# Optimization experiments

Hardware: AMD Instinct MI355X
Metric: run time of the kernel (lower is better)

## Reference

```python
import jax, jax.numpy as jnp
import numpy as np

B, H, M = 8192, 1024, 4096


def setup_inputs() -> dict:
    key = jax.random.key(0)
    ks = jax.random.split(key, 5)
    s = 1.0 / np.sqrt(H)  # keep projections well-scaled
    return {
        "x": jax.random.normal(ks[0], (B, H), dtype=jnp.float32),
        "memory_bank": jax.random.normal(ks[1], (M, H), dtype=jnp.float32),
        "Wq": jax.random.normal(ks[2], (H, H), dtype=jnp.float32) * s,
        "bq": jnp.zeros((H,), dtype=jnp.float32),
        "Wk": jax.random.normal(ks[3], (H, H), dtype=jnp.float32) * s,
        "bk": jnp.zeros((H,), dtype=jnp.float32),
        "Wv": jax.random.normal(ks[4], (H, H), dtype=jnp.float32) * s,
        "bv": jnp.zeros((H,), dtype=jnp.float32),
    }


def reference(x, memory_bank, Wq, bq, Wk, bk, Wv, bv):
    # Dense projections (Keras Dense: y = x @ W + b)
    query = x @ Wq + bq                    # [B, H]
    keys = memory_bank @ Wk + bk           # [M, H]
    values = memory_bank @ Wv + bv         # [M, H]
    d_k = jnp.asarray(keys.shape[-1], dtype=query.dtype)
    scores = (query @ keys.T) / jnp.sqrt(d_k)   # [B, M]
    weights = jax.nn.softmax(scores, axis=-1)   # softmax over memory slots
    memory_context = weights @ values           # [B, H]
    return x + memory_context
```

## Files before the change

kernel.cpp:

```cpp
#include <hip/hip_runtime.h>
#include <stdint.h>

typedef unsigned short u16;
typedef unsigned char u8;
using f32x4 = __attribute__((ext_vector_type(4))) float;
using i32x4 = __attribute__((ext_vector_type(4))) int;
using i32x8 = __attribute__((ext_vector_type(8))) int;

__device__ __forceinline__ void gload_lds16(const void* g, void* l) {
  __builtin_amdgcn_global_load_lds(
      (const __attribute__((address_space(1))) void*)g,
      (__attribute__((address_space(3))) void*)l, 16, 0, 0);
}

#define DSRO(dst, base, offbytes) \
  asm volatile("ds_read_b128 %0, %1 offset:%2" : "=v"(dst) : "v"(base), "i"(offbytes))

__device__ __forceinline__ u8 f2fp8(float v) {
  return (u8)((uint32_t)__builtin_amdgcn_cvt_pk_fp8_f32(v, 0.f, 0, false) & 0xff);
}

__global__ __launch_bounds__(256) void cast_fp8_kernel(
    const float* __restrict__ in, u8* __restrict__ out, int n8) {
  int idx = blockIdx.x * blockDim.x + threadIdx.x;
  int stride = gridDim.x * blockDim.x;
  for (int i = idx; i < n8; i += stride) {
    const float4* p = (const float4*)(in + (size_t)i * 8);
    float4 a = p[0], b = p[1];
    uint32_t w0 = (uint32_t)__builtin_amdgcn_cvt_pk_fp8_f32(a.x, a.y, 0, false);
    w0 = (uint32_t)__builtin_amdgcn_cvt_pk_fp8_f32(a.z, a.w, (int)w0, true);
    uint32_t w1 = (uint32_t)__builtin_amdgcn_cvt_pk_fp8_f32(b.x, b.y, 0, false);
    w1 = (uint32_t)__builtin_amdgcn_cvt_pk_fp8_f32(b.z, b.w, (int)w1, true);
    uint2 o; o.x = w0; o.y = w1;
    *(uint2*)(out + (size_t)i * 8) = o;
  }
}

__global__ __launch_bounds__(256) void tcast_fp8_kernel(
    const float* __restrict__ W, u8* __restrict__ Wt, int Kd, int Nd) {
  __shared__ u8 tile[32][33];
  int nbx = Nd / 32;
  int bx = blockIdx.x % nbx;
  int by = blockIdx.x / nbx;
  int tr = threadIdx.x >> 5;
  int tc = threadIdx.x & 31;
#pragma unroll
  for (int i = 0; i < 4; ++i)
    tile[tr + i * 8][tc] = f2fp8(W[(size_t)(by * 32 + tr + i * 8) * Nd + bx * 32 + tc]);
  __syncthreads();
#pragma unroll
  for (int i = 0; i < 4; ++i)
    Wt[(size_t)(bx * 32 + tr + i * 8) * Kd + by * 32 + tc] = tile[tc][tr + i * 8];
}

#define GATE0 asm volatile("s_waitcnt vmcnt(0)" ::: "memory")
#define LGKM0 asm volatile("s_waitcnt lgkmcnt(0)" ::: "memory")
#define SBARA asm volatile("s_barrier" ::: "memory")
#define SCHED0 __builtin_amdgcn_sched_barrier(0)
#define NOSTG (void)0
#define NOTAIL (void)0
#define TAIL_G0 do { GATE0; SBARA; } while (0)

#define PVSTG(buf, kt) do { \
    const u8* sa_ = Asrc + (size_t)(kt) * 128; \
    gload_lds16(sa_,                    &As8[buf][wave * 1024]); \
    gload_lds16(sa_ + (size_t)64 * Kd,  &As8[buf][wave * 1024 + 8192]); \
    gload_lds16(sa_ + (size_t)128 * Kd, &As8[buf][wave * 1024 + 16384]); \
    gload_lds16(sa_ + (size_t)192 * Kd, &As8[buf][wave * 1024 + 24576]); \
    const u8* sb_ = Bsrc + (size_t)(kt) * 128; \
    gload_lds16(sb_,                    &Bs8[buf][wave * 1024]); \
    gload_lds16(sb_ + (size_t)64 * Kd,  &Bs8[buf][wave * 1024 + 8192]); \
  } while (0)

#define PVPH(buf, STAGE, TAIL) do { \
    i32x4 alo[4], ahi[4], blo[4], bhi[4]; \
    _Pragma("unroll") \
    for (int q = 0; q < 4; ++q) { \
      DSRO(alo[q], pvA[buf], q * 2048); \
      DSRO(ahi[q], pvA2[buf], q * 2048); \
      DSRO(blo[q], pvB[buf], q * 2048); \
      DSRO(bhi[q], pvB2[buf], q * 2048); \
    } \
    STAGE; \
    LGKM0; \
    SCHED0; \
    __builtin_amdgcn_s_setprio(1); \
    _Pragma("unroll") \
    for (int i2 = 0; i2 < 4; ++i2) { \
      i32x8 av = __builtin_shufflevector(alo[i2], ahi[i2], 0, 1, 2, 3, 4, 5, 6, 7); \
      _Pragma("unroll") \
      for (int j2 = 0; j2 < 4; ++j2) { \
        i32x8 bv = __builtin_shufflevector(blo[j2], bhi[j2], 0, 1, 2, 3, 4, 5, 6, 7); \
        acc[i2][j2] = __builtin_amdgcn_mfma_scale_f32_16x16x128_f8f6f4( \
            av, bv, acc[i2][j2], 0, 0, 0, 127, 0, 127); \
      } \
    } \
    __builtin_amdgcn_s_setprio(0); \
    SCHED0; \
    TAIL; \
  } while (0)

#define FP8GEMM_SETUP \
  int tid = threadIdx.x; \
  int lane = tid & 63; \
  int wave = tid >> 6; \
  int wm = (wave >> 1) * 64; \
  int wn = (wave & 1) * 64; \
  int laneh = lane & 15; \
  int lanev = lane >> 4; \
  int prow = tid >> 3; \
  int lslot = (tid & 7) ^ (prow & 7); \
  const u8* Asrc = A + (m0 + prow) * Kd + lslot * 16; \
  const u8* Bsrc = Bt + (n0 + prow) * Kd + lslot * 16; \
  int arow = wm + laneh; \
  int brow = wn + laneh; \
  uint32_t pvA[2], pvA2[2], pvB[2], pvB2[2]; \
  _Pragma("unroll") \
  for (int b = 0; b < 2; ++b) { \
    pvA[b]  = (uint32_t)(uintptr_t)&As8[b][arow * 128 + (((2 * lanev) ^ (arow & 7)) * 16)]; \
    pvA2[b] = (uint32_t)(uintptr_t)&As8[b][arow * 128 + (((2 * lanev + 1) ^ (arow & 7)) * 16)]; \
    pvB[b]  = (uint32_t)(uintptr_t)&Bs8[b][brow * 128 + (((2 * lanev) ^ (brow & 7)) * 16)]; \
    pvB2[b] = (uint32_t)(uintptr_t)&Bs8[b][brow * 128 + (((2 * lanev + 1) ^ (brow & 7)) * 16)]; \
  }

#define FP8GEMM_MAIN \
  PVSTG(0, 0); \
  GATE0; \
  SBARA; \
  int NI = Kd >> 7; \
  for (int it = 0; it < (NI >> 1) - 1; ++it) { \
    PVPH(0, PVSTG(1, 2 * it + 1), TAIL_G0); \
    PVPH(1, PVSTG(0, 2 * it + 2), TAIL_G0); \
  } \
  PVPH(0, PVSTG(1, NI - 1), TAIL_G0); \
  PVPH(1, NOSTG, NOTAIL);

#define EPI_FP8_FLAT(DST, BIAS) do { \
    int crow = (int)m0 + wm + (lanev << 2); \
    int ccol = (int)n0 + wn + laneh; \
    _Pragma("unroll") \
    for (int mi = 0; mi < 4; ++mi) \
      _Pragma("unroll") \
      for (int r = 0; r < 4; ++r) { \
        size_t row = (size_t)(crow + mi * 16 + r); \
        float v0 = acc[mi][0][r] + BIAS[ccol]; \
        float v1 = acc[mi][1][r] + BIAS[ccol + 16]; \
        float v2 = acc[mi][2][r] + BIAS[ccol + 32]; \
        float v3 = acc[mi][3][r] + BIAS[ccol + 48]; \
        uint32_t p01 = (uint32_t)__builtin_amdgcn_cvt_pk_fp8_f32(v0, v1, 0, false); \
        uint32_t p23 = (uint32_t)__builtin_amdgcn_cvt_pk_fp8_f32(v2, v3, 0, false); \
        size_t base = row * N + ccol; \
        DST[base]      = (u8)(p01 & 0xff); \
        DST[base + 16] = (u8)((p01 >> 8) & 0xff); \
        DST[base + 32] = (u8)(p23 & 0xff); \
        DST[base + 48] = (u8)((p23 >> 8) & 0xff); \
      } \
  } while (0)

__global__ __launch_bounds__(512, 2) void gemm_q8(
    const u8* __restrict__ A, const u8* __restrict__ Bt, u8* __restrict__ C,
    const float* __restrict__ bias, int M, int N, int Kd) {
  __shared__ u8 As8[2][256 * 128];
  __shared__ u8 Bs8[2][128 * 128];

  int bid = blockIdx.x;
  int bm = (bid & 7) * 4 + ((bid >> 3) & 3);
  int bn = bid >> 5;
  size_t m0 = (size_t)bm << 8;
  size_t n0 = (size_t)bn << 7;

  FP8GEMM_SETUP
  f32x4 acc[4][4] = {};
  FP8GEMM_MAIN
  EPI_FP8_FLAT(C, bias);
}

__global__ __launch_bounds__(512, 2) void gemm_kv8(
    const u8* __restrict__ mb8, const u8* __restrict__ Wkt8,
    const u8* __restrict__ Wvt8, u8* __restrict__ K8, u8* __restrict__ Vt8,
    const float* __restrict__ bk, const float* __restrict__ bv,
    int M, int N, int Kd) {
  __shared__ u8 As8[2][256 * 128];
  __shared__ u8 Bs8[2][128 * 128];

  int bid = blockIdx.x;
  int role = bid >> 7;
  int local = bid & 127;
  int bm = local & 15;
  int bn = local >> 4;
  size_t m0 = (size_t)bm << 8;
  size_t n0 = (size_t)bn << 7;

  const u8* A = mb8;
  const u8* Bt = role ? Wvt8 : Wkt8;

  FP8GEMM_SETUP
  f32x4 acc[4][4] = {};
  FP8GEMM_MAIN

  if (role == 0) {
    EPI_FP8_FLAT(K8, bk);
  } else {
    int crow = (int)m0 + wm + (lanev << 2);
    int ccol = (int)n0 + wn + laneh;
#pragma unroll
    for (int ni = 0; ni < 4; ++ni) {
      float b = bv[ccol + ni * 16];
#pragma unroll
      for (int mi = 0; mi < 4; ++mi) {
        uint32_t w = (uint32_t)__builtin_amdgcn_cvt_pk_fp8_f32(
            acc[mi][ni][0] + b, acc[mi][ni][1] + b, 0, false);
        w = (uint32_t)__builtin_amdgcn_cvt_pk_fp8_f32(
            acc[mi][ni][2] + b, acc[mi][ni][3] + b, (int)w, true);
        *(uint32_t*)&Vt8[(size_t)(ccol + ni * 16) * M + crow + mi * 16] = w;
      }
    }
  }
}

__global__ __launch_bounds__(512, 2) void gemm_qkt8(
    const u8* __restrict__ A, const u8* __restrict__ Bt, u8* __restrict__ C,
    float* __restrict__ sums, int M, int N, int Kd) {
  __shared__ u8 As8[2][256 * 128];
  __shared__ u8 Bs8[2][128 * 128];

  int bid = blockIdx.x;
  int bm = (bid & 7) * 4 + ((bid >> 3) & 3);
  int bn = bid >> 5;
  size_t m0 = (size_t)bm << 8;
  size_t n0 = (size_t)bn << 7;

  FP8GEMM_SETUP
  f32x4 acc[4][4] = {};
  FP8GEMM_MAIN

  SBARA;

  u8* epw = ((u8*)As8) + wave * 4608;
  int gcol0 = (int)n0 + wn;
#pragma unroll
  for (int mi = 0; mi < 4; ++mi)
#pragma unroll
    for (int r = 0; r < 4; ++r) {
      int rowL = mi * 16 + lanev * 4 + r;
      float e0 = __expf(acc[mi][0][r] * 0.03125f);
      float e1 = __expf(acc[mi][1][r] * 0.03125f);
      float e2 = __expf(acc[mi][2][r] * 0.03125f);
      float e3 = __expf(acc[mi][3][r] * 0.03125f);
      uint32_t p01 = (uint32_t)__builtin_amdgcn_cvt_pk_fp8_f32(e0, e1, 0, false);
      uint32_t p23 = (uint32_t)__builtin_amdgcn_cvt_pk_fp8_f32(e2, e3, 0, false);
      int base = rowL * 72 + laneh;
      epw[base]      = (u8)(p01 & 0xff);
      epw[base + 16] = (u8)((p01 >> 8) & 0xff);
      epw[base + 32] = (u8)(p23 & 0xff);
      epw[base + 48] = (u8)((p23 >> 8) & 0xff);
    }
#pragma unroll
  for (int p = 0; p < 4; ++p) {
    int rowL = (lane >> 2) + 16 * p;
    uint4 v = *(const uint4*)&epw[rowL * 72 + (lane & 3) * 16];
    size_t grow = m0 + wm + rowL;
    *(uint4*)&C[grow * N + gcol0 + (lane & 3) * 16] = v;
    float s = 0.f;
    s += __builtin_amdgcn_cvt_f32_fp8((int)v.x, 0);
    s += __builtin_amdgcn_cvt_f32_fp8((int)v.x, 1);
    s += __builtin_amdgcn_cvt_f32_fp8((int)v.x, 2);
    s += __builtin_amdgcn_cvt_f32_fp8((int)v.x, 3);
    s += __builtin_amdgcn_cvt_f32_fp8((int)v.y, 0);
    s += __builtin_amdgcn_cvt_f32_fp8((int)v.y, 1);
    s += __builtin_amdgcn_cvt_f32_fp8((int)v.y, 2);
    s += __builtin_amdgcn_cvt_f32_fp8((int)v.y, 3);
    s += __builtin_amdgcn_cvt_f32_fp8((int)v.z, 0);
    s += __builtin_amdgcn_cvt_f32_fp8((int)v.z, 1);
    s += __builtin_amdgcn_cvt_f32_fp8((int)v.z, 2);
    s += __builtin_amdgcn_cvt_f32_fp8((int)v.z, 3);
    s += __builtin_amdgcn_cvt_f32_fp8((int)v.w, 0);
    s += __builtin_amdgcn_cvt_f32_fp8((int)v.w, 1);
    s += __builtin_amdgcn_cvt_f32_fp8((int)v.w, 2);
    s += __builtin_amdgcn_cvt_f32_fp8((int)v.w, 3);
    s += __shfl_xor(s, 1, 64);
    s += __shfl_xor(s, 2, 64);
    if ((lane & 3) == 0) atomicAdd(&sums[grow], s);
  }
}

__global__ __launch_bounds__(512, 2) void gemm_pv_fp8(
    const u8* __restrict__ A, const u8* __restrict__ Bt,
    float* __restrict__ C, const float* __restrict__ sums,
    const float* __restrict__ xres, int M, int N, int Kd) {
  __shared__ u8 As8[2][256 * 128];
  __shared__ u8 Bs8[2][128 * 128];

  int bid = blockIdx.x;
  int bm = (bid & 7) * 4 + ((bid >> 3) & 3);
  int bn = bid >> 5;
  size_t m0 = (size_t)bm << 8;
  size_t n0 = (size_t)bn << 7;

  FP8GEMM_SETUP
  f32x4 acc[4][4] = {};
  FP8GEMM_MAIN

  int crow = (int)m0 + wm + (lanev << 2);
  int ccol = (int)n0 + wn + laneh;
#pragma unroll
  for (int mi = 0; mi < 4; ++mi)
#pragma unroll
    for (int r = 0; r < 4; ++r) {
      int row = crow + mi * 16 + r;
      float inv = 1.0f / sums[row];
      size_t rbase = (size_t)row * N + ccol;
#pragma unroll
      for (int ni = 0; ni < 4; ++ni)
        C[rbase + ni * 16] = xres[rbase + ni * 16] + acc[mi][ni][r] * inv;
    }
}

extern "C" void kernel_launch(void* const* d_in, const int* in_sizes, int n_in,
                              void* d_out, int out_size, void* d_ws, size_t ws_size,
                              hipStream_t stream) {
  const float* x  = (const float*)d_in[0];
  const float* mb = (const float*)d_in[1];
  const float* Wq = (const float*)d_in[2];
  const float* bq = (const float*)d_in[3];
  const float* Wk = (const float*)d_in[4];
  const float* bk = (const float*)d_in[5];
  const float* Wv = (const float*)d_in[6];
  const float* bv = (const float*)d_in[7];
  float* out = (float*)d_out;

  const int B = 8192, H = 1024, Mm = 4096;

  char* ws = (char*)d_ws;
  u8* x8   = (u8*)ws; ws += (size_t)B * H;
  u8* mb8  = (u8*)ws; ws += (size_t)Mm * H;
  u8* Wqt8 = (u8*)ws; ws += (size_t)H * H;
  u8* Wkt8 = (u8*)ws; ws += (size_t)H * H;
  u8* Wvt8 = (u8*)ws; ws += (size_t)H * H;
  u8* Q8   = (u8*)ws; ws += (size_t)B * H;
  u8* K8   = (u8*)ws; ws += (size_t)Mm * H;
  u8* Vt8  = (u8*)ws; ws += (size_t)H * Mm;
  u8* S8   = (u8*)ws; ws += (size_t)B * Mm;
  float* sums = (float*)ws;

  (void)hipMemsetAsync(sums, 0, (size_t)B * sizeof(float), stream);

  cast_fp8_kernel<<<2048, 256, 0, stream>>>(x, x8, B * H / 8);
  cast_fp8_kernel<<<1024, 256, 0, stream>>>(mb, mb8, Mm * H / 8);
  tcast_fp8_kernel<<<(H / 32) * (H / 32), 256, 0, stream>>>(Wq, Wqt8, H, H);
  tcast_fp8_kernel<<<(H / 32) * (H / 32), 256, 0, stream>>>(Wk, Wkt8, H, H);
  tcast_fp8_kernel<<<(H / 32) * (H / 32), 256, 0, stream>>>(Wv, Wvt8, H, H);

  gemm_q8<<<(B / 256) * (H / 128), 512, 0, stream>>>(x8, Wqt8, Q8, bq, B, H, H);
  gemm_kv8<<<2 * (Mm / 256) * (H / 128), 512, 0, stream>>>(
      mb8, Wkt8, Wvt8, K8, Vt8, bk, bv, Mm, H, H);

  gemm_qkt8<<<(B / 256) * (Mm / 128), 512, 0, stream>>>(Q8, K8, S8, sums, B, Mm, H);

  gemm_pv_fp8<<<(B / 256) * (H / 128), 512, 0, stream>>>(S8, Vt8, out, sums, x, B, H, Mm);
}
```

Measured before the change: 141.5 us.

## Replace QK^T and PV GEMMs with simpler 128x128 single-buffered FP8 kernels

Replaces the 256x128 double-buffered, hand-scheduled FP8 GEMMs for scores and PV with new 128x128-tile, 256-thread kernels. The new kernels use one LDS buffer with XOR-swizzled loads and two __syncthreads per K step, plus a different block-swizzle order. This raises block count and occupancy but gives up the explicit load/compute overlap and the larger per-block reuse of the previous pipeline.

```diff
diff --git a/kernel.cpp b/kernel.cpp
--- a/kernel.cpp
+++ b/kernel.cpp
@@ -60,6 +60,164 @@
 #define NOSTG (void)0
 #define NOTAIL (void)0
 #define TAIL_G0 do { GATE0; SBARA; } while (0)
+
+
+#define FP8C_SETUP \
+  int tid = threadIdx.x; \
+  int lane = tid & 63; \
+  int wave = tid >> 6; \
+  int wm = (wave >> 1) * 64; \
+  int wn = (wave & 1) * 64; \
+  int laneh = lane & 15; \
+  int lanev = lane >> 4; \
+  int srow = wave * 8 + (lane >> 3); \
+  int sslot = (lane & 7) ^ (lane >> 3); \
+  const u8* Asrc = A + (m0 + srow) * Kd + sslot * 16; \
+  const u8* Bsrc = Bt + (n0 + srow) * Kd + sslot * 16; \
+  int arow = wm + laneh; \
+  int brow = wn + laneh; \
+  u8* Asm = smem; \
+  u8* Bsm = smem + 16384;
+
+#define STG128(kt) do { \
+    const u8* sa_ = Asrc + (size_t)(kt) * 128; \
+    gload_lds16(sa_,                   Asm + wave * 1024); \
+    gload_lds16(sa_ + (size_t)32 * Kd, Asm + wave * 1024 + 4096); \
+    gload_lds16(sa_ + (size_t)64 * Kd, Asm + wave * 1024 + 8192); \
+    gload_lds16(sa_ + (size_t)96 * Kd, Asm + wave * 1024 + 12288); \
+    const u8* sb_ = Bsrc + (size_t)(kt) * 128; \
+    gload_lds16(sb_,                   Bsm + wave * 1024); \
+    gload_lds16(sb_ + (size_t)32 * Kd, Bsm + wave * 1024 + 4096); \
+    gload_lds16(sb_ + (size_t)64 * Kd, Bsm + wave * 1024 + 8192); \
+    gload_lds16(sb_ + (size_t)96 * Kd, Bsm + wave * 1024 + 12288); \
+  } while (0)
+
+#define FP8C_COMPUTE do { \
+    i32x4 alo[4], ahi[4], blo[4], bhi[4]; \
+    _Pragma("unroll") \
+    for (int q = 0; q < 4; ++q) { \
+      int ar = arow + q * 16, br = brow + q * 16; \
+      alo[q] = *(const i32x4*)&Asm[ar * 128 + (((2 * lanev)     ^ (ar & 7)) * 16)]; \
+      ahi[q] = *(const i32x4*)&Asm[ar * 128 + (((2 * lanev + 1) ^ (ar & 7)) * 16)]; \
+      blo[q] = *(const i32x4*)&Bsm[br * 128 + (((2 * lanev)     ^ (br & 7)) * 16)]; \
+      bhi[q] = *(const i32x4*)&Bsm[br * 128 + (((2 * lanev + 1) ^ (br & 7)) * 16)]; \
+    } \
+    _Pragma("unroll") \
+    for (int i2 = 0; i2 < 4; ++i2) { \
+      i32x8 av = __builtin_shufflevector(alo[i2], ahi[i2], 0, 1, 2, 3, 4, 5, 6, 7); \
+      _Pragma("unroll") \
+      for (int j2 = 0; j2 < 4; ++j2) { \
+        i32x8 bv = __builtin_shufflevector(blo[j2], bhi[j2], 0, 1, 2, 3, 4, 5, 6, 7); \
+        acc[i2][j2] = __builtin_amdgcn_mfma_scale_f32_16x16x128_f8f6f4( \
+            av, bv, acc[i2][j2], 0, 0, 0, 127, 0, 127); \
+      } \
+    } \
+  } while (0)
+
+#define FP8C_MAIN \
+  int NI = Kd >> 7; \
+  for (int kt = 0; kt < NI; ++kt) { \
+    STG128(kt); \
+    __syncthreads(); \
+    FP8C_COMPUTE; \
+    __syncthreads(); \
+  }
+
+__global__ __launch_bounds__(256) void qkt8_128(
+    const u8* __restrict__ A, const u8* __restrict__ Bt, u8* __restrict__ C,
+    float* __restrict__ sums, int M, int N, int Kd) {
+  __shared__ u8 smem[32768];
+
+  int bid = blockIdx.x;
+  int swz = (bid & 7) * 256 + (bid >> 3);
+  int bm = swz & 63;
+  int bn = swz >> 6;
+  size_t m0 = (size_t)bm << 7;
+  size_t n0 = (size_t)bn << 7;
+
+  FP8C_SETUP
+  f32x4 acc[4][4] = {};
+  FP8C_MAIN
+
+  u8* epw = smem + wave * 4608;
+  int gcol0 = (int)n0 + wn;
+#pragma unroll
+  for (int mi = 0; mi < 4; ++mi)
+#pragma unroll
+    for (int r = 0; r < 4; ++r) {
+      int rowL = mi * 16 + lanev * 4 + r;
+      float e0 = __expf(acc[mi][0][r] * 0.03125f);
+      float e1 = __expf(acc[mi][1][r] * 0.03125f);
+      float e2 = __expf(acc[mi][2][r] * 0.03125f);
+      float e3 = __expf(acc[mi][3][r] * 0.03125f);
+      uint32_t p01 = (uint32_t)__builtin_amdgcn_cvt_pk_fp8_f32(e0, e1, 0, false);
+      uint32_t p23 = (uint32_t)__builtin_amdgcn_cvt_pk_fp8_f32(e2, e3, 0, false);
+      int base = rowL * 72 + laneh;
+      epw[base]      = (u8)(p01 & 0xff);
+      epw[base + 16] = (u8)((p01 >> 8) & 0xff);
+      epw[base + 32] = (u8)(p23 & 0xff);
+      epw[base + 48] = (u8)((p23 >> 8) & 0xff);
+    }
+#pragma unroll
+  for (int p = 0; p < 4; ++p) {
+    int rowL = (lane >> 2) + 16 * p;
+    uint4 v = *(const uint4*)&epw[rowL * 72 + (lane & 3) * 16];
+    size_t grow = m0 + wm + rowL;
+    *(uint4*)&C[grow * N + gcol0 + (lane & 3) * 16] = v;
+    float s = 0.f;
+    s += __builtin_amdgcn_cvt_f32_fp8((int)v.x, 0);
+    s += __builtin_amdgcn_cvt_f32_fp8((int)v.x, 1);
+    s += __builtin_amdgcn_cvt_f32_fp8((int)v.x, 2);
+    s += __builtin_amdgcn_cvt_f32_fp8((int)v.x, 3);
+    s += __builtin_amdgcn_cvt_f32_fp8((int)v.y, 0);
+    s += __builtin_amdgcn_cvt_f32_fp8((int)v.y, 1);
+    s += __builtin_amdgcn_cvt_f32_fp8((int)v.y, 2);
+    s += __builtin_amdgcn_cvt_f32_fp8((int)v.y, 3);
+    s += __builtin_amdgcn_cvt_f32_fp8((int)v.z, 0);
+    s += __builtin_amdgcn_cvt_f32_fp8((int)v.z, 1);
+    s += __builtin_amdgcn_cvt_f32_fp8((int)v.z, 2);
+    s += __builtin_amdgcn_cvt_f32_fp8((int)v.z, 3);
+    s += __builtin_amdgcn_cvt_f32_fp8((int)v.w, 0);
+    s += __builtin_amdgcn_cvt_f32_fp8((int)v.w, 1);
+    s += __builtin_amdgcn_cvt_f32_fp8((int)v.w, 2);
+    s += __builtin_amdgcn_cvt_f32_fp8((int)v.w, 3);
+    s += __shfl_xor(s, 1, 64);
+    s += __shfl_xor(s, 2, 64);
+    if ((lane & 3) == 0) atomicAdd(&sums[grow], s);
+  }
+}
+
+__global__ __launch_bounds__(256) void pv8_128(
+    const u8* __restrict__ A, const u8* __restrict__ Bt,
+    float* __restrict__ C, const float* __restrict__ sums,
+    const float* __restrict__ xres, int M, int N, int Kd) {
+  __shared__ u8 smem[32768];
+
+  int bid = blockIdx.x;
+  int swz = (bid & 7) * 64 + (bid >> 3);
+  int bm = swz & 63;
+  int bn = swz >> 6;
+  size_t m0 = (size_t)bm << 7;
+  size_t n0 = (size_t)bn << 7;
+
+  FP8C_SETUP
+  f32x4 acc[4][4] = {};
+  FP8C_MAIN
+
+  int crow = (int)m0 + wm + (lanev << 2);
+  int ccol = (int)n0 + wn + laneh;
+#pragma unroll
+  for (int mi = 0; mi < 4; ++mi)
+#pragma unroll
+    for (int r = 0; r < 4; ++r) {
+      int row = crow + mi * 16 + r;
+      float inv = 1.0f / sums[row];
+      size_t rbase = (size_t)row * N + ccol;
+#pragma unroll
+      for (int ni = 0; ni < 4; ++ni)
+        C[rbase + ni * 16] = xres[rbase + ni * 16] + acc[mi][ni][r] * inv;
+    }
+}
 
 #define PVSTG(buf, kt) do { \
     const u8* sa_ = Asrc + (size_t)(kt) * 128; \
@@ -218,104 +376,6 @@
   }
 }
 
-__global__ __launch_bounds__(512, 2) void gemm_qkt8(
-    const u8* __restrict__ A, const u8* __restrict__ Bt, u8* __restrict__ C,
-    float* __restrict__ sums, int M, int N, int Kd) {
-  __shared__ u8 As8[2][256 * 128];
-  __shared__ u8 Bs8[2][128 * 128];
-
-  int bid = blockIdx.x;
-  int bm = (bid & 7) * 4 + ((bid >> 3) & 3);
-  int bn = bid >> 5;
-  size_t m0 = (size_t)bm << 8;
-  size_t n0 = (size_t)bn << 7;
-
-  FP8GEMM_SETUP
-  f32x4 acc[4][4] = {};
-  FP8GEMM_MAIN
-
-  SBARA;
-
-  u8* epw = ((u8*)As8) + wave * 4608;
-  int gcol0 = (int)n0 + wn;
-#pragma unroll
-  for (int mi = 0; mi < 4; ++mi)
-#pragma unroll
-    for (int r = 0; r < 4; ++r) {
-      int rowL = mi * 16 + lanev * 4 + r;
-      float e0 = __expf(acc[mi][0][r] * 0.03125f);
-      float e1 = __expf(acc[mi][1][r] * 0.03125f);
-      float e2 = __expf(acc[mi][2][r] * 0.03125f);
-      float e3 = __expf(acc[mi][3][r] * 0.03125f);
-      uint32_t p01 = (uint32_t)__builtin_amdgcn_cvt_pk_fp8_f32(e0, e1, 0, false);
-      uint32_t p23 = (uint32_t)__builtin_amdgcn_cvt_pk_fp8_f32(e2, e3, 0, false);
-      int base = rowL * 72 + laneh;
-      epw[base]      = (u8)(p01 & 0xff);
-      epw[base + 16] = (u8)((p01 >> 8) & 0xff);
-      epw[base + 32] = (u8)(p23 & 0xff);
-      epw[base + 48] = (u8)((p23 >> 8) & 0xff);
-    }
-#pragma unroll
-  for (int p = 0; p < 4; ++p) {
-    int rowL = (lane >> 2) + 16 * p;
-    uint4 v = *(const uint4*)&epw[rowL * 72 + (lane & 3) * 16];
-    size_t grow = m0 + wm + rowL;
-    *(uint4*)&C[grow * N + gcol0 + (lane & 3) * 16] = v;
-    float s = 0.f;
-    s += __builtin_amdgcn_cvt_f32_fp8((int)v.x, 0);
-    s += __builtin_amdgcn_cvt_f32_fp8((int)v.x, 1);
-    s += __builtin_amdgcn_cvt_f32_fp8((int)v.x, 2);
-    s += __builtin_amdgcn_cvt_f32_fp8((int)v.x, 3);
-    s += __builtin_amdgcn_cvt_f32_fp8((int)v.y, 0);
-    s += __builtin_amdgcn_cvt_f32_fp8((int)v.y, 1);
-    s += __builtin_amdgcn_cvt_f32_fp8((int)v.y, 2);
-    s += __builtin_amdgcn_cvt_f32_fp8((int)v.y, 3);
-    s += __builtin_amdgcn_cvt_f32_fp8((int)v.z, 0);
-    s += __builtin_amdgcn_cvt_f32_fp8((int)v.z, 1);
-    s += __builtin_amdgcn_cvt_f32_fp8((int)v.z, 2);
-    s += __builtin_amdgcn_cvt_f32_fp8((int)v.z, 3);
-    s += __builtin_amdgcn_cvt_f32_fp8((int)v.w, 0);
-    s += __builtin_amdgcn_cvt_f32_fp8((int)v.w, 1);
-    s += __builtin_amdgcn_cvt_f32_fp8((int)v.w, 2);
-    s += __builtin_amdgcn_cvt_f32_fp8((int)v.w, 3);
-    s += __shfl_xor(s, 1, 64);
-    s += __shfl_xor(s, 2, 64);
-    if ((lane & 3) == 0) atomicAdd(&sums[grow], s);
-  }
-}
-
-__global__ __launch_bounds__(512, 2) void gemm_pv_fp8(
-    const u8* __restrict__ A, const u8* __restrict__ Bt,
-    float* __restrict__ C, const float* __restrict__ sums,
-    const float* __restrict__ xres, int M, int N, int Kd) {
-  __shared__ u8 As8[2][256 * 128];
-  __shared__ u8 Bs8[2][128 * 128];
-
-  int bid = blockIdx.x;
-  int bm = (bid & 7) * 4 + ((bid >> 3) & 3);
-  int bn = bid >> 5;
-  size_t m0 = (size_t)bm << 8;
-  size_t n0 = (size_t)bn << 7;
-
-  FP8GEMM_SETUP
-  f32x4 acc[4][4] = {};
-  FP8GEMM_MAIN
-
-  int crow = (int)m0 + wm + (lanev << 2);
-  int ccol = (int)n0 + wn + laneh;
-#pragma unroll
-  for (int mi = 0; mi < 4; ++mi)
-#pragma unroll
-    for (int r = 0; r < 4; ++r) {
-      int row = crow + mi * 16 + r;
-      float inv = 1.0f / sums[row];
-      size_t rbase = (size_t)row * N + ccol;
-#pragma unroll
-      for (int ni = 0; ni < 4; ++ni)
-        C[rbase + ni * 16] = xres[rbase + ni * 16] + acc[mi][ni][r] * inv;
-    }
-}
-
 extern "C" void kernel_launch(void* const* d_in, const int* in_sizes, int n_in,
                               void* d_out, int out_size, void* d_ws, size_t ws_size,
                               hipStream_t stream) {
@@ -355,7 +415,7 @@
   gemm_kv8<<<2 * (Mm / 256) * (H / 128), 512, 0, stream>>>(
       mb8, Wkt8, Wvt8, K8, Vt8, bk, bv, Mm, H, H);
 
-  gemm_qkt8<<<(B / 256) * (Mm / 128), 512, 0, stream>>>(Q8, K8, S8, sums, B, Mm, H);
-
-  gemm_pv_fp8<<<(B / 256) * (H / 128), 512, 0, stream>>>(S8, Vt8, out, sums, x, B, H, Mm);
-}
+  qkt8_128<<<(B / 128) * (Mm / 128), 256, 0, stream>>>(Q8, K8, S8, sums, B, Mm, H);
+
+  pv8_128<<<(B / 128) * (H / 128), 256, 0, stream>>>(S8, Vt8, out, sums, x, B, H, Mm);
+}
```

After: 151.9 us. 1.07x slower.
